# Optimization experiments

Measured on AMD Instinct MI355X. Metric: run time of the kernel, lower is better.

## Reference

```python
import jax, jax.numpy as jnp
import numpy as np

NUM_HEADS = 8
NUM_LEVELS = 4
NUM_POINTS = 4
EMBED = 256
OFFSET_SCALE = 1.0
SPATIAL = [(96, 96), (48, 48), (24, 24), (12, 12)]  # (H_l, W_l) per level


def _grid_sample_bilinear(fmap, grid):
    """fmap: (N, C, H, W); grid: (N, Q, K, 2) with (x, y) in [-1, 1].
    Bilinear, align_corners=True. Locations are pre-clamped to [-1,1] so
    index clipping reproduces torch zeros-padding behavior exactly."""
    N, C, H, W = fmap.shape
    x = (grid[..., 0] + 1.0) * 0.5 * (W - 1)
    y = (grid[..., 1] + 1.0) * 0.5 * (H - 1)
    x0 = jnp.floor(x)
    y0 = jnp.floor(y)
    wx = (x - x0)[:, None]  # (N,1,Q,K)
    wy = (y - y0)[:, None]
    x0i = jnp.clip(x0.astype(jnp.int32), 0, W - 1)
    x1i = jnp.clip(x0i + 1, 0, W - 1)
    y0i = jnp.clip(y0.astype(jnp.int32), 0, H - 1)
    y1i = jnp.clip(y0i + 1, 0, H - 1)
    flat = fmap.reshape(N, C, H * W)
    Q, K = grid.shape[1], grid.shape[2]

    def g(yi, xi):
        idx = (yi * W + xi).reshape(N, 1, Q * K)
        return jnp.take_along_axis(flat, idx, axis=2).reshape(N, C, Q, K)

    return ((1 - wy) * ((1 - wx) * g(y0i, x0i) + wx * g(y0i, x1i))
            + wy * ((1 - wx) * g(y1i, x0i) + wx * g(y1i, x1i)))


def setup_inputs() -> dict:
    key = jax.random.key(0)
    ks = jax.random.split(key, 8)
    B, Q, E = 2, 12240, EMBED
    H, L, K = NUM_HEADS, NUM_LEVELS, NUM_POINTS
    Vlen = sum(h * w for h, w in SPATIAL)
    s = 0.02
    queries = jax.random.normal(ks[0], (B, Q, E), jnp.float32)
    ref_points = 2.0 * jax.random.uniform(ks[1], (B, Q, L, 2), jnp.float32) - 1.0
    value = jax.random.normal(ks[2], (B, Vlen, E), jnp.float32)
    Wv = jax.random.normal(ks[3], (E, E), jnp.float32) * s
    Woff = jax.random.normal(ks[4], (E, H * L * K * 2), jnp.float32) * s
    boff = jnp.zeros((H * L * K * 2,), jnp.float32)
    Wattn = jax.random.normal(ks[5], (E, H * L * K), jnp.float32) * s
    battn = jnp.zeros((H * L * K,), jnp.float32)
    Wout = jax.random.normal(ks[6], (E, E), jnp.float32) * s
    vss = jnp.array(SPATIAL, dtype=jnp.int32)
    return {"queries": queries, "ref_points": ref_points, "value": value,
            "Wv": Wv, "Woff": Woff, "boff": boff, "Wattn": Wattn,
            "battn": battn, "Wout": Wout, "value_spatial_shapes": vss}


def _forward(queries, ref_points, value, Wv, Woff, boff, Wattn, battn, Wout, spatial):
    B, Q, E = queries.shape
    H, L, K = NUM_HEADS, NUM_LEVELS, NUM_POINTS
    hd = E // H
    Vlen = value.shape[1]
    # offsets MLP (tanh) and attention weights
    offsets = OFFSET_SCALE * jnp.tanh(queries @ Woff + boff)
    offsets = offsets.reshape(B, Q, H, L, K, 2)
    attn = jax.nn.softmax((queries @ Wattn + battn).reshape(B, Q, H, L * K), axis=-1)
    attn = attn.reshape(B, Q, H, L, K).transpose(0, 2, 3, 1, 4).reshape(B * H, L, Q, K)
    # value projection -> (B*H, head_dim, Vlen)
    v = (value @ Wv).reshape(B, Vlen, H, hd).transpose(0, 2, 3, 1).reshape(B * H, hd, Vlen)
    # sampling locations (B*H, L, Q, K, 2)
    locs = jnp.clip(ref_points[:, :, None, :, None, :] + offsets, -1.0, 1.0)
    locs = locs.transpose(0, 2, 3, 1, 4, 5).reshape(B * H, L, Q, K, 2)
    # per-level bilinear sample + weighted accumulate
    sizes = [h * w for h, w in spatial]
    starts = np.concatenate([[0], np.cumsum(sizes)])
    acc = jnp.zeros((B * H, hd, Q, K), jnp.float32)
    for lvl, (Hl, Wl) in enumerate(spatial):
        fmap = v[:, :, starts[lvl]:starts[lvl + 1]].reshape(B * H, hd, Hl, Wl)
        samp = _grid_sample_bilinear(fmap, locs[:, lvl])  # (B*H, hd, Q, K)
        acc = acc + samp * attn[:, lvl][:, None]
    out = acc.reshape(B, E, Q, K).transpose(0, 2, 1, 3).sum(axis=-1)  # (B, Q, E)
    return out @ Wout


def reference(queries, ref_points, value, Wv, Woff, boff, Wattn, battn, Wout, value_spatial_shapes):
    spatial = [tuple(int(x) for x in row) for row in np.asarray(value_spatial_shapes)]
    return _forward(queries, ref_points, value, Wv, Woff, boff, Wattn, battn, Wout, spatial)
```

## Files before the change

kernel.cpp:

```cpp
#include <hip/hip_runtime.h>
#include <math.h>

#define NB 2
#define NQ 12240
#define NH 8
#define NL 4
#define NK 4
#define VLEN 12240
#define M_TOT (NB * NQ)
#define MT (M_TOT / 16)
#define FRAG_A (MT * 8 * 64)

typedef __attribute__((ext_vector_type(4))) float f32x4;
typedef __attribute__((ext_vector_type(8))) short bf16x8;
typedef __attribute__((ext_vector_type(8))) unsigned short u16x8;

__device__ __forceinline__ ushort f2bf(float x) {
    union { float f; unsigned u; } v; v.f = x;
    unsigned r = v.u + 0x7fffu + ((v.u >> 16) & 1u);
    return (ushort)(r >> 16);
}
__device__ __forceinline__ float bf2f(ushort h) {
    union { unsigned u; float f; } v; v.u = ((unsigned)h) << 16; return v.f;
}

__global__ __launch_bounds__(256) void preconv_all(
    const float* __restrict__ Q, const float* __restrict__ V,
    const float* __restrict__ Woff, const float* __restrict__ Wattn,
    const float* __restrict__ Wv,   const float* __restrict__ Wout,
    ushort* __restrict__ QAh, ushort* __restrict__ QAl,
    ushort* __restrict__ VAh, ushort* __restrict__ Bp)
{
    const int g = blockIdx.x * 256 + threadIdx.x;
    if (g < 2 * FRAG_A) {
        const bool isQ = (g < FRAG_A);
        const int t = isQ ? g : g - FRAG_A;
        const float* X = isQ ? Q : V;
        const int l = t & 63;
        const int kt = (t >> 6) & 7;
        const int mt = t >> 9;
        const int row = mt * 16 + (l & 15);
        const int col = kt * 32 + ((l >> 4) << 3);
        const float* src = X + (size_t)row * 256 + col;
        float4 a0 = *(const float4*)src;
        float4 a1 = *(const float4*)(src + 4);
        ushort4 h0, h1;
        h0.x = f2bf(a0.x); h0.y = f2bf(a0.y); h0.z = f2bf(a0.z); h0.w = f2bf(a0.w);
        h1.x = f2bf(a1.x); h1.y = f2bf(a1.y); h1.z = f2bf(a1.z); h1.w = f2bf(a1.w);
        ushort* H = isQ ? QAh : VAh;
        *(ushort4*)(H + (size_t)t * 8)     = h0;
        *(ushort4*)(H + (size_t)t * 8 + 4) = h1;
        if (isQ) {
            ushort4 l0, l1;
            l0.x = f2bf(a0.x - bf2f(h0.x)); l0.y = f2bf(a0.y - bf2f(h0.y));
            l0.z = f2bf(a0.z - bf2f(h0.z)); l0.w = f2bf(a0.w - bf2f(h0.w));
            l1.x = f2bf(a1.x - bf2f(h1.x)); l1.y = f2bf(a1.y - bf2f(h1.y));
            l1.z = f2bf(a1.z - bf2f(h1.z)); l1.w = f2bf(a1.w - bf2f(h1.w));
            *(ushort4*)(QAl + (size_t)t * 8)     = l0;
            *(ushort4*)(QAl + (size_t)t * 8 + 4) = l1;
        }
    } else {
        const int gg = g - 2 * FRAG_A;
        const float* W; ushort* H; ushort* L; int N, tl;
        if (gg < 8192)       { W = Woff;  H = Bp + 0;      L = Bp + 98304;  N = 256; tl = gg; }
        else if (gg < 12288) { W = Wattn; H = Bp + 65536;  L = Bp + 163840; N = 128; tl = gg - 8192; }
        else if (gg < 20480) { W = Wv;    H = Bp + 196608; L = Bp + 262144; N = 256; tl = gg - 12288; }
        else                 { W = Wout;  H = Bp + 327680; L = Bp + 393216; N = 256; tl = gg - 20480; }
        const int l  = tl & 63;
        const int kt = (tl >> 6) & 7;
        const int nt = tl >> 9;
        const int colb = nt * 16 + (l & 15);
        const int krow = kt * 32 + ((l >> 4) << 3);
        ushort h8[8], l8[8];
        #pragma unroll
        for (int j = 0; j < 8; ++j) {
            float x = W[(size_t)(krow + j) * N + colb];
            h8[j] = f2bf(x);
            l8[j] = f2bf(x - bf2f(h8[j]));
        }
        *(ushort4*)(H + (size_t)tl * 8)     = *(ushort4*)&h8[0];
        *(ushort4*)(H + (size_t)tl * 8 + 4) = *(ushort4*)&h8[4];
        *(ushort4*)(L + (size_t)tl * 8)     = *(ushort4*)&l8[0];
        *(ushort4*)(L + (size_t)tl * 8 + 4) = *(ushort4*)&l8[4];
    }
}

template<int TERMS, int EPI>
__global__ __launch_bounds__(384) void gemm_frag(
    const ushort* __restrict__ Ah, const ushort* __restrict__ Al,
    const ushort* __restrict__ Bh, const ushort* __restrict__ Bl,
    const float* __restrict__ bias, const float* __restrict__ bias2,
    const float* __restrict__ ref,
    void* __restrict__ C0, void* __restrict__ C1)
{
    const int wave = threadIdx.x >> 6;
    const int lane = threadIdx.x & 63;
    const int mt   = blockIdx.x;
    const int nt0  = wave * 4;

    f32x4 acc[4] = {};
    const ushort* aH = Ah + ((size_t)mt * 8 * 64 + lane) * 8;
    const ushort* aL = (TERMS == 3) ? Al + ((size_t)mt * 8 * 64 + lane) * 8 : nullptr;

    #pragma unroll
    for (int kt = 0; kt < 8; ++kt) {
        bf16x8 ah = *(const bf16x8*)(aH + kt * 512);
        bf16x8 al;
        if (TERMS == 3) al = *(const bf16x8*)(aL + kt * 512);
        bf16x8 bh[4], bl[4];
        #pragma unroll
        for (int fn = 0; fn < 4; ++fn) {
            size_t off = (((size_t)(nt0 + fn) * 8 + kt) * 64 + lane) * 8;
            bh[fn] = *(const bf16x8*)(Bh + off);
            if (TERMS >= 2) bl[fn] = *(const bf16x8*)(Bl + off);
        }
        #pragma unroll
        for (int fn = 0; fn < 4; ++fn) {
            acc[fn] = __builtin_amdgcn_mfma_f32_16x16x32_bf16(ah, bh[fn], acc[fn], 0, 0, 0);
            if (TERMS >= 2)
                acc[fn] = __builtin_amdgcn_mfma_f32_16x16x32_bf16(ah, bl[fn], acc[fn], 0, 0, 0);
            if (TERMS == 3)
                acc[fn] = __builtin_amdgcn_mfma_f32_16x16x32_bf16(al, bh[fn], acc[fn], 0, 0, 0);
        }
    }

    const int lr = lane & 15, r0 = (lane >> 4) * 4;
    const int rowb = mt * 16 + r0;

    if (EPI == 0) {
        if (wave < 4) {
            #pragma unroll
            for (int fn = 0; fn < 4; ++fn) {
                const int c  = wave * 64 + fn * 16 + lr;
                const int l  = (c >> 3) & 3;
                const int xy = c & 1;
                const float sc = 0.5f * (float)(96 >> l) - 0.5f;
                const float b = bias[c];
                #pragma unroll
                for (int r = 0; r < 4; ++r) {
                    const int row = rowb + r;
                    const float rp = ref[(size_t)row * 8 + l * 2 + xy];
                    const float t  = tanhf(acc[fn][r] + b);
                    const float lc = fminf(fmaxf(rp + t, -1.f), 1.f);
                    ((float*)C0)[(size_t)row * 256 + c] = (lc + 1.f) * sc;
                }
            }
        } else {
            #pragma unroll
            for (int fn = 0; fn < 4; ++fn) {
                const int hcol = (wave - 4) * 64 + fn * 16 + lr;
                const float b = bias2[hcol];
                #pragma unroll
                for (int r = 0; r < 4; ++r) {
                    float e = expf(acc[fn][r] + b);
                    float s = e;
                    s += __shfl_xor(s, 1);
                    s += __shfl_xor(s, 2);
                    s += __shfl_xor(s, 4);
                    s += __shfl_xor(s, 8);
                    ((float*)C1)[(size_t)(rowb + r) * 128 + hcol] = e / s;
                }
            }
        }
    } else if (EPI == 1) {
        #pragma unroll
        for (int fn = 0; fn < 4; ++fn) {
            const int col = (nt0 + fn) * 16 + lr;
            #pragma unroll
            for (int r = 0; r < 4; ++r)
                ((ushort*)C0)[(size_t)(rowb + r) * 256 + col] = f2bf(acc[fn][r]);
        }
    } else {
        #pragma unroll
        for (int fn = 0; fn < 4; ++fn) {
            const int col = (nt0 + fn) * 16 + lr;
            #pragma unroll
            for (int r = 0; r < 4; ++r)
                ((float*)C0)[(size_t)(rowb + r) * 256 + col] = acc[fn][r];
        }
    }
}

__global__ __launch_bounds__(256, 5) void sample_kernel(
    const ushort* __restrict__ v_bf,
    const float* __restrict__ locs,
    const float* __restrict__ attnw,
    ushort* __restrict__ AccH)
{
    __shared__ float sloc[64][36];
    __shared__ float satt[64][20];

    const int h   = blockIdx.x & 7;
    const int qc  = blockIdx.x >> 3;
    const int tid = threadIdx.x;

    #pragma unroll
    for (int i = 0; i < 2; ++i) {
        int idx = tid + i * 256;
        int row = idx >> 3;
        int c   = (idx & 7) * 4;
        int bqr = qc * 64 + row;
        float4 v = make_float4(0.f, 0.f, 0.f, 0.f);
        if (bqr < M_TOT) v = *(const float4*)(locs + (size_t)bqr * 256 + h * 32 + c);
        *(float4*)&sloc[row][c] = v;
    }
    {
        int row = tid >> 2;
        int c   = (tid & 3) * 4;
        int bqr = qc * 64 + row;
        float4 v = make_float4(0.f, 0.f, 0.f, 0.f);
        if (bqr < M_TOT) v = *(const float4*)(attnw + (size_t)bqr * 128 + h * 16 + c);
        *(float4*)&satt[row][c] = v;
    }
    __syncthreads();

    const int qi = tid >> 2;
    const int c8 = tid & 3;
    const int bq = qc * 64 + qi;
    const int b  = (bq >= NQ) ? 1 : 0;
    const ushort* vbase = v_bf + ((size_t)b * VLEN) * 256 + h * 32 + c8 * 8;

    float acc[8] = {};
    #pragma unroll
    for (int l = 0; l < NL; ++l) {
        const int Wl = 96 >> l;
        const int st = (l == 0) ? 0 : (l == 1) ? 9216 : (l == 2) ? 11520 : 12096;
        #pragma unroll 2
        for (int k = 0; k < NK; ++k) {
            float px = sloc[qi][(l * 4 + k) * 2 + 0];
            float py = sloc[qi][(l * 4 + k) * 2 + 1];
            float w  = satt[qi][l * 4 + k];
            float x0f = floorf(px), y0f = floorf(py);
            float wx = px - x0f, wy = py - y0f;
            int x0 = (int)x0f, y0 = (int)y0f;
            x0 = min(max(x0, 0), Wl - 1);
            y0 = min(max(y0, 0), Wl - 1);
            int x1 = min(x0 + 1, Wl - 1);
            int y1 = min(y0 + 1, Wl - 1);
            float w11 = w * wy * wx;
            float w10 = w * wy - w11;
            float w01 = w * wx - w11;
            float w00 = w - w01 - w10 - w11;
            const ushort* r0 = vbase + (size_t)(st + y0 * Wl) * 256;
            const ushort* r1 = vbase + (size_t)(st + y1 * Wl) * 256;
            u16x8 u00 = *(const u16x8*)(r0 + (size_t)x0 * 256);
            u16x8 u01 = *(const u16x8*)(r0 + (size_t)x1 * 256);
            u16x8 u10 = *(const u16x8*)(r1 + (size_t)x0 * 256);
            u16x8 u11 = *(const u16x8*)(r1 + (size_t)x1 * 256);
            #pragma unroll
            for (int j = 0; j < 8; ++j) {
                acc[j] += w00 * bf2f(u00[j]) + w01 * bf2f(u01[j])
                        + w10 * bf2f(u10[j]) + w11 * bf2f(u11[j]);
            }
        }
    }

    if (bq < M_TOT) {
        const int mt  = bq >> 4;
        const int lfr = (c8 << 4) | (bq & 15);
        const size_t base = (((size_t)mt * 8 + h) * 64 + lfr) * 8;
        u16x8 hh;
        #pragma unroll
        for (int j = 0; j < 8; ++j) hh[j] = f2bf(acc[j]);
        *(u16x8*)(AccH + base) = hh;
    }
}

extern "C" void kernel_launch(void* const* d_in, const int* in_sizes, int n_in,
                              void* d_out, int out_size, void* d_ws, size_t ws_size,
                              hipStream_t stream)
{
    const float* queries = (const float*)d_in[0];
    const float* refpts  = (const float*)d_in[1];
    const float* value   = (const float*)d_in[2];
    const float* Wv      = (const float*)d_in[3];
    const float* Woff    = (const float*)d_in[4];
    const float* boff    = (const float*)d_in[5];
    const float* Wattn   = (const float*)d_in[6];
    const float* battn   = (const float*)d_in[7];
    const float* Wout    = (const float*)d_in[8];
    float* out = (float*)d_out;

    char* ws = (char*)d_ws;
    float*  off_ws  = (float*)(ws);
    float*  attn_ws = (float*)(ws + 25067520);
    ushort* v_bf    = (ushort*)(ws + 37601280);
    ushort* QAh     = (ushort*)(ws + 50135040);
    ushort* QAl     = (ushort*)(ws + 62668800);
    ushort* VAh     = (ushort*)(ws + 75202560);
    ushort* Bp      = (ushort*)(ws + 87736320);

    preconv_all<<<6232, 256, 0, stream>>>(queries, value, Woff, Wattn, Wv, Wout,
                                          QAh, QAl, VAh, Bp);
    gemm_frag<3, 0><<<1530, 384, 0, stream>>>(QAh, QAl, Bp, Bp + 98304,
                                              boff, battn, refpts, off_ws, attn_ws);
    gemm_frag<1, 1><<<1530, 256, 0, stream>>>(VAh, nullptr, Bp + 196608, nullptr,
                                              nullptr, nullptr, nullptr, v_bf, nullptr);
    sample_kernel<<<3064, 256, 0, stream>>>(v_bf, off_ws, attn_ws, QAh);
    gemm_frag<2, 2><<<1530, 256, 0, stream>>>(QAh, nullptr, Bp + 327680, Bp + 393216,
                                              nullptr, nullptr, nullptr, out, nullptr);
}
```

Measured before the change: 227.0 us.

## Fuse fp32-to-bf16 activation conversion into GEMMs and merge Q/V projection launches

```diff
diff --git a/kernel.cpp b/kernel.cpp
--- a/kernel.cpp
+++ b/kernel.cpp
@@ -9,7 +9,6 @@
 #define VLEN 12240
 #define M_TOT (NB * NQ)
 #define MT (M_TOT / 16)
-#define FRAG_A (MT * 8 * 64)
 
 typedef __attribute__((ext_vector_type(4))) float f32x4;
 typedef __attribute__((ext_vector_type(8))) short bf16x8;
@@ -24,110 +23,90 @@
     union { unsigned u; float f; } v; v.u = ((unsigned)h) << 16; return v.f;
 }
 
-__global__ __launch_bounds__(256) void preconv_all(
-    const float* __restrict__ Q, const float* __restrict__ V,
+__global__ __launch_bounds__(256) void preconv_B(
     const float* __restrict__ Woff, const float* __restrict__ Wattn,
     const float* __restrict__ Wv,   const float* __restrict__ Wout,
-    ushort* __restrict__ QAh, ushort* __restrict__ QAl,
-    ushort* __restrict__ VAh, ushort* __restrict__ Bp)
-{
-    const int g = blockIdx.x * 256 + threadIdx.x;
-    if (g < 2 * FRAG_A) {
-        const bool isQ = (g < FRAG_A);
-        const int t = isQ ? g : g - FRAG_A;
-        const float* X = isQ ? Q : V;
-        const int l = t & 63;
-        const int kt = (t >> 6) & 7;
-        const int mt = t >> 9;
-        const int row = mt * 16 + (l & 15);
-        const int col = kt * 32 + ((l >> 4) << 3);
-        const float* src = X + (size_t)row * 256 + col;
-        float4 a0 = *(const float4*)src;
-        float4 a1 = *(const float4*)(src + 4);
-        ushort4 h0, h1;
-        h0.x = f2bf(a0.x); h0.y = f2bf(a0.y); h0.z = f2bf(a0.z); h0.w = f2bf(a0.w);
-        h1.x = f2bf(a1.x); h1.y = f2bf(a1.y); h1.z = f2bf(a1.z); h1.w = f2bf(a1.w);
-        ushort* H = isQ ? QAh : VAh;
-        *(ushort4*)(H + (size_t)t * 8)     = h0;
-        *(ushort4*)(H + (size_t)t * 8 + 4) = h1;
-        if (isQ) {
-            ushort4 l0, l1;
-            l0.x = f2bf(a0.x - bf2f(h0.x)); l0.y = f2bf(a0.y - bf2f(h0.y));
-            l0.z = f2bf(a0.z - bf2f(h0.z)); l0.w = f2bf(a0.w - bf2f(h0.w));
-            l1.x = f2bf(a1.x - bf2f(h1.x)); l1.y = f2bf(a1.y - bf2f(h1.y));
-            l1.z = f2bf(a1.z - bf2f(h1.z)); l1.w = f2bf(a1.w - bf2f(h1.w));
-            *(ushort4*)(QAl + (size_t)t * 8)     = l0;
-            *(ushort4*)(QAl + (size_t)t * 8 + 4) = l1;
-        }
-    } else {
-        const int gg = g - 2 * FRAG_A;
-        const float* W; ushort* H; ushort* L; int N, tl;
-        if (gg < 8192)       { W = Woff;  H = Bp + 0;      L = Bp + 98304;  N = 256; tl = gg; }
-        else if (gg < 12288) { W = Wattn; H = Bp + 65536;  L = Bp + 163840; N = 128; tl = gg - 8192; }
-        else if (gg < 20480) { W = Wv;    H = Bp + 196608; L = Bp + 262144; N = 256; tl = gg - 12288; }
-        else                 { W = Wout;  H = Bp + 327680; L = Bp + 393216; N = 256; tl = gg - 20480; }
-        const int l  = tl & 63;
-        const int kt = (tl >> 6) & 7;
-        const int nt = tl >> 9;
-        const int colb = nt * 16 + (l & 15);
-        const int krow = kt * 32 + ((l >> 4) << 3);
-        ushort h8[8], l8[8];
-        #pragma unroll
-        for (int j = 0; j < 8; ++j) {
-            float x = W[(size_t)(krow + j) * N + colb];
-            h8[j] = f2bf(x);
-            l8[j] = f2bf(x - bf2f(h8[j]));
-        }
-        *(ushort4*)(H + (size_t)tl * 8)     = *(ushort4*)&h8[0];
-        *(ushort4*)(H + (size_t)tl * 8 + 4) = *(ushort4*)&h8[4];
-        *(ushort4*)(L + (size_t)tl * 8)     = *(ushort4*)&l8[0];
-        *(ushort4*)(L + (size_t)tl * 8 + 4) = *(ushort4*)&l8[4];
-    }
-}
-
-template<int TERMS, int EPI>
-__global__ __launch_bounds__(384) void gemm_frag(
-    const ushort* __restrict__ Ah, const ushort* __restrict__ Al,
-    const ushort* __restrict__ Bh, const ushort* __restrict__ Bl,
+    ushort* __restrict__ Bp)
+{
+    const int gg = blockIdx.x * 256 + threadIdx.x;
+    const float* W; ushort* H; ushort* L; int N, tl;
+    if (gg < 8192)       { W = Woff;  H = Bp + 0;      L = Bp + 98304;  N = 256; tl = gg; }
+    else if (gg < 12288) { W = Wattn; H = Bp + 65536;  L = Bp + 163840; N = 128; tl = gg - 8192; }
+    else if (gg < 20480) { W = Wv;    H = Bp + 196608; L = Bp + 262144; N = 256; tl = gg - 12288; }
+    else                 { W = Wout;  H = Bp + 327680; L = Bp + 393216; N = 256; tl = gg - 20480; }
+    const int l  = tl & 63;
+    const int kt = (tl >> 6) & 7;
+    const int nt = tl >> 9;
+    const int colb = nt * 16 + (l & 15);
+    const int krow = kt * 32 + ((l >> 4) << 3);
+    ushort h8[8], l8[8];
+    #pragma unroll
+    for (int j = 0; j < 8; ++j) {
+        float x = W[(size_t)(krow + j) * N + colb];
+        h8[j] = f2bf(x);
+        l8[j] = f2bf(x - bf2f(h8[j]));
+    }
+    *(ushort4*)(H + (size_t)tl * 8)     = *(ushort4*)&h8[0];
+    *(ushort4*)(H + (size_t)tl * 8 + 4) = *(ushort4*)&h8[4];
+    *(ushort4*)(L + (size_t)tl * 8)     = *(ushort4*)&l8[0];
+    *(ushort4*)(L + (size_t)tl * 8 + 4) = *(ushort4*)&l8[4];
+}
+
+__global__ __launch_bounds__(384) void gemm_qv(
+    const float* __restrict__ Qf, const float* __restrict__ Vf,
+    const ushort* __restrict__ Bp,
     const float* __restrict__ bias, const float* __restrict__ bias2,
     const float* __restrict__ ref,
-    void* __restrict__ C0, void* __restrict__ C1)
+    float* __restrict__ locC, float* __restrict__ attC,
+    ushort* __restrict__ vC)
 {
     const int wave = threadIdx.x >> 6;
     const int lane = threadIdx.x & 63;
-    const int mt   = blockIdx.x;
-    const int nt0  = wave * 4;
+    const bool isV = (blockIdx.x >= MT);
+    const int mt   = isV ? (blockIdx.x - MT) : blockIdx.x;
+    if (isV && wave >= 4) return;
+    const int nt0 = wave * 4;
+    const int lr = lane & 15, r0g = (lane >> 4) * 4;
+    const int rowb = mt * 16 + r0g;
+
+    const float* Af = (isV ? Vf : Qf) + (size_t)(mt * 16 + lr) * 256 + ((lane >> 4) << 3);
 
     f32x4 acc[4] = {};
-    const ushort* aH = Ah + ((size_t)mt * 8 * 64 + lane) * 8;
-    const ushort* aL = (TERMS == 3) ? Al + ((size_t)mt * 8 * 64 + lane) * 8 : nullptr;
-
-    #pragma unroll
-    for (int kt = 0; kt < 8; ++kt) {
-        bf16x8 ah = *(const bf16x8*)(aH + kt * 512);
-        bf16x8 al;
-        if (TERMS == 3) al = *(const bf16x8*)(aL + kt * 512);
-        bf16x8 bh[4], bl[4];
-        #pragma unroll
-        for (int fn = 0; fn < 4; ++fn) {
-            size_t off = (((size_t)(nt0 + fn) * 8 + kt) * 64 + lane) * 8;
-            bh[fn] = *(const bf16x8*)(Bh + off);
-            if (TERMS >= 2) bl[fn] = *(const bf16x8*)(Bl + off);
-        }
-        #pragma unroll
-        for (int fn = 0; fn < 4; ++fn) {
-            acc[fn] = __builtin_amdgcn_mfma_f32_16x16x32_bf16(ah, bh[fn], acc[fn], 0, 0, 0);
-            if (TERMS >= 2)
-                acc[fn] = __builtin_amdgcn_mfma_f32_16x16x32_bf16(ah, bl[fn], acc[fn], 0, 0, 0);
-            if (TERMS == 3)
-                acc[fn] = __builtin_amdgcn_mfma_f32_16x16x32_bf16(al, bh[fn], acc[fn], 0, 0, 0);
-        }
-    }
-
-    const int lr = lane & 15, r0 = (lane >> 4) * 4;
-    const int rowb = mt * 16 + r0;
-
-    if (EPI == 0) {
+
+    if (!isV) {
+        const ushort* BH = Bp;
+        const ushort* BL = Bp + 98304;
+        #pragma unroll
+        for (int kt = 0; kt < 8; ++kt) {
+            float4 a0 = *(const float4*)(Af + kt * 32);
+            float4 a1 = *(const float4*)(Af + kt * 32 + 4);
+            union { bf16x8 v; ushort u[8]; } ah, al;
+            #pragma unroll
+            for (int j = 0; j < 4; ++j) {
+                float x = (&a0.x)[j];
+                ushort hv = f2bf(x);
+                ah.u[j] = hv; al.u[j] = f2bf(x - bf2f(hv));
+            }
+            #pragma unroll
+            for (int j = 0; j < 4; ++j) {
+                float x = (&a1.x)[j];
+                ushort hv = f2bf(x);
+                ah.u[4 + j] = hv; al.u[4 + j] = f2bf(x - bf2f(hv));
+            }
+            bf16x8 bh[4], bl[4];
+            #pragma unroll
+            for (int fn = 0; fn < 4; ++fn) {
+                size_t off = (((size_t)(nt0 + fn) * 8 + kt) * 64 + lane) * 8;
+                bh[fn] = *(const bf16x8*)(BH + off);
+                bl[fn] = *(const bf16x8*)(BL + off);
+            }
+            #pragma unroll
+            for (int fn = 0; fn < 4; ++fn) {
+                acc[fn] = __builtin_amdgcn_mfma_f32_16x16x32_bf16(ah.v, bh[fn], acc[fn], 0, 0, 0);
+                acc[fn] = __builtin_amdgcn_mfma_f32_16x16x32_bf16(ah.v, bl[fn], acc[fn], 0, 0, 0);
+                acc[fn] = __builtin_amdgcn_mfma_f32_16x16x32_bf16(al.v, bh[fn], acc[fn], 0, 0, 0);
+            }
+        }
         if (wave < 4) {
             #pragma unroll
             for (int fn = 0; fn < 4; ++fn) {
@@ -142,7 +121,7 @@
                     const float rp = ref[(size_t)row * 8 + l * 2 + xy];
                     const float t  = tanhf(acc[fn][r] + b);
                     const float lc = fminf(fmaxf(rp + t, -1.f), 1.f);
-                    ((float*)C0)[(size_t)row * 256 + c] = (lc + 1.f) * sc;
+                    locC[(size_t)row * 256 + c] = (lc + 1.f) * sc;
                 }
             }
         } else {
@@ -158,30 +137,42 @@
                     s += __shfl_xor(s, 2);
                     s += __shfl_xor(s, 4);
                     s += __shfl_xor(s, 8);
-                    ((float*)C1)[(size_t)(rowb + r) * 128 + hcol] = e / s;
+                    attC[(size_t)(rowb + r) * 128 + hcol] = e / s;
                 }
             }
         }
-    } else if (EPI == 1) {
+    } else {
+        const ushort* BH = Bp + 196608;
+        #pragma unroll
+        for (int kt = 0; kt < 8; ++kt) {
+            float4 a0 = *(const float4*)(Af + kt * 32);
+            float4 a1 = *(const float4*)(Af + kt * 32 + 4);
+            union { bf16x8 v; ushort u[8]; } ah;
+            #pragma unroll
+            for (int j = 0; j < 4; ++j) ah.u[j]     = f2bf((&a0.x)[j]);
+            #pragma unroll
+            for (int j = 0; j < 4; ++j) ah.u[4 + j] = f2bf((&a1.x)[j]);
+            bf16x8 bh[4];
+            #pragma unroll
+            for (int fn = 0; fn < 4; ++fn) {
+                size_t off = (((size_t)(nt0 + fn) * 8 + kt) * 64 + lane) * 8;
+                bh[fn] = *(const bf16x8*)(BH + off);
+            }
+            #pragma unroll
+            for (int fn = 0; fn < 4; ++fn)
+                acc[fn] = __builtin_amdgcn_mfma_f32_16x16x32_bf16(ah.v, bh[fn], acc[fn], 0, 0, 0);
+        }
         #pragma unroll
         for (int fn = 0; fn < 4; ++fn) {
             const int col = (nt0 + fn) * 16 + lr;
             #pragma unroll
             for (int r = 0; r < 4; ++r)
-                ((ushort*)C0)[(size_t)(rowb + r) * 256 + col] = f2bf(acc[fn][r]);
-        }
-    } else {
-        #pragma unroll
-        for (int fn = 0; fn < 4; ++fn) {
-            const int col = (nt0 + fn) * 16 + lr;
-            #pragma unroll
-            for (int r = 0; r < 4; ++r)
-                ((float*)C0)[(size_t)(rowb + r) * 256 + col] = acc[fn][r];
-        }
-    }
-}
-
-__global__ __launch_bounds__(256, 5) void sample_kernel(
+                vC[(size_t)(rowb + r) * 256 + col] = f2bf(acc[fn][r]);
+        }
+    }
+}
+
+__global__ __launch_bounds__(256) void sample_kernel(
     const ushort* __restrict__ v_bf,
     const float* __restrict__ locs,
     const float* __restrict__ attnw,
@@ -225,7 +216,7 @@
     for (int l = 0; l < NL; ++l) {
         const int Wl = 96 >> l;
         const int st = (l == 0) ? 0 : (l == 1) ? 9216 : (l == 2) ? 11520 : 12096;
-        #pragma unroll 2
+        #pragma unroll
         for (int k = 0; k < NK; ++k) {
             float px = sloc[qi][(l * 4 + k) * 2 + 0];
             float py = sloc[qi][(l * 4 + k) * 2 + 1];
@@ -266,6 +257,47 @@
     }
 }
 
+__global__ __launch_bounds__(256) void gemm_out(
+    const ushort* __restrict__ Ah,
+    const ushort* __restrict__ Bh, const ushort* __restrict__ Bl,
+    float* __restrict__ C)
+{
+    const int wave = threadIdx.x >> 6;
+    const int lane = threadIdx.x & 63;
+    const int mt   = blockIdx.x;
+    const int nt0  = wave * 4;
+
+    f32x4 acc[4] = {};
+    const ushort* aH = Ah + ((size_t)mt * 8 * 64 + lane) * 8;
+
+    #pragma unroll
+    for (int kt = 0; kt < 8; ++kt) {
+        bf16x8 ah = *(const bf16x8*)(aH + kt * 512);
+        bf16x8 bh[4], bl[4];
+        #pragma unroll
+        for (int fn = 0; fn < 4; ++fn) {
+            size_t off = (((size_t)(nt0 + fn) * 8 + kt) * 64 + lane) * 8;
+            bh[fn] = *(const bf16x8*)(Bh + off);
+            bl[fn] = *(const bf16x8*)(Bl + off);
+        }
+        #pragma unroll
+        for (int fn = 0; fn < 4; ++fn) {
+            acc[fn] = __builtin_amdgcn_mfma_f32_16x16x32_bf16(ah, bh[fn], acc[fn], 0, 0, 0);
+            acc[fn] = __builtin_amdgcn_mfma_f32_16x16x32_bf16(ah, bl[fn], acc[fn], 0, 0, 0);
+        }
+    }
+
+    const int lr = lane & 15, r0 = (lane >> 4) * 4;
+    const int rowb = mt * 16 + r0;
+    #pragma unroll
+    for (int fn = 0; fn < 4; ++fn) {
+        const int col = (nt0 + fn) * 16 + lr;
+        #pragma unroll
+        for (int r = 0; r < 4; ++r)
+            C[(size_t)(rowb + r) * 256 + col] = acc[fn][r];
+    }
+}
+
 extern "C" void kernel_launch(void* const* d_in, const int* in_sizes, int n_in,
                               void* d_out, int out_size, void* d_ws, size_t ws_size,
                               hipStream_t stream)
@@ -285,18 +317,12 @@
     float*  off_ws  = (float*)(ws);
     float*  attn_ws = (float*)(ws + 25067520);
     ushort* v_bf    = (ushort*)(ws + 37601280);
-    ushort* QAh     = (ushort*)(ws + 50135040);
-    ushort* QAl     = (ushort*)(ws + 62668800);
-    ushort* VAh     = (ushort*)(ws + 75202560);
+    ushort* AccH    = (ushort*)(ws + 50135040);
     ushort* Bp      = (ushort*)(ws + 87736320);
 
-    preconv_all<<<6232, 256, 0, stream>>>(queries, value, Woff, Wattn, Wv, Wout,
-                                          QAh, QAl, VAh, Bp);
-    gemm_frag<3, 0><<<1530, 384, 0, stream>>>(QAh, QAl, Bp, Bp + 98304,
-                                              boff, battn, refpts, off_ws, attn_ws);
-    gemm_frag<1, 1><<<1530, 256, 0, stream>>>(VAh, nullptr, Bp + 196608, nullptr,
-                                              nullptr, nullptr, nullptr, v_bf, nullptr);
-    sample_kernel<<<3064, 256, 0, stream>>>(v_bf, off_ws, attn_ws, QAh);
-    gemm_frag<2, 2><<<1530, 256, 0, stream>>>(QAh, nullptr, Bp + 327680, Bp + 393216,
-                                              nullptr, nullptr, nullptr, out, nullptr);
-}
+    preconv_B<<<112, 256, 0, stream>>>(Woff, Wattn, Wv, Wout, Bp);
+    gemm_qv<<<3060, 384, 0, stream>>>(queries, value, Bp, boff, battn, refpts,
+                                      off_ws, attn_ws, v_bf);
+    sample_kernel<<<3064, 256, 0, stream>>>(v_bf, off_ws, attn_ws, AccH);
+    gemm_out<<<1530, 256, 0, stream>>>(AccH, Bp + 327680, Bp + 393216, out);
+}
```

Result: no change. 231.1 us (+1.8%).
